# Kernel optimization log

Measured on AMD Instinct MI355X. Metric: run time of the kernel, lower is better.

## Reference

```python
import jax, jax.numpy as jnp
import numpy as np

B, S, D, E, H, TOP_K = 8, 2048, 512, 10, 2048, 2

def setup_inputs() -> dict:
    key = jax.random.key(0)
    ks = jax.random.split(key, 8)
    sd = 0.02
    return {
        "x": jax.random.normal(ks[0], (B, S, D), jnp.float32),
        "noise": jax.random.normal(ks[1], (B, S, E), jnp.float32),
        "Wr": jax.random.normal(ks[2], (D, E), jnp.float32) * sd,
        "br": jnp.zeros((E,), jnp.float32),
        "Wn": jax.random.normal(ks[3], (D, E), jnp.float32) * sd,
        "bn": jnp.zeros((E,), jnp.float32),
        "W1": jax.random.normal(ks[4], (E, D, H), jnp.float32) * sd,
        "b1": jnp.zeros((E, H), jnp.float32),
        "W2": jax.random.normal(ks[5], (E, H, D), jnp.float32) * sd,
        "b2": jnp.zeros((E, D), jnp.float32),
    }

def reference(x, noise, Wr, br, Wn, bn, W1, b1, W2, b2):
    # Noisy top-k router
    logits = x @ Wr + br                                  # [B,S,E]
    noise_logits = x @ Wn + bn                            # [B,S,E]
    noisy = logits + noise * jax.nn.softplus(noise_logits)
    top_vals, top_idx = jax.lax.top_k(noisy, TOP_K)       # [B,S,k]
    # softmax over -inf-scattered logits == softmax over top-k values scattered back
    g_topk = jax.nn.softmax(top_vals, axis=-1)            # [B,S,k]
    n_exp = Wr.shape[-1]
    gating = jnp.sum(jax.nn.one_hot(top_idx, n_exp, dtype=x.dtype) * g_topk[..., None], axis=-2)  # [B,S,E]
    # Dense combine: gating is exactly zero for unselected experts, so weighting
    # every expert's FFN output reproduces the masked gather/scatter loop.
    out = jnp.zeros_like(x)
    for e in range(n_exp):  # small fixed expert count
        h = jax.nn.relu(x @ W1[e] + b1[e])                # [B,S,H]
        y = h @ W2[e] + b2[e]                             # [B,S,D]
        out = out + gating[..., e:e+1] * y
    return out
```

## Files before the change

### kernel.cpp

```cpp
#include <hip/hip_runtime.h>
#include <hip/hip_bf16.h>
#include <stdint.h>


#define N_TOK 16384
#define DIM 512
#define NEXP 10
#define HID 2048
#define BM 128
#define BN 128
#define BK 64
#define MAXSLOT (2*N_TOK + NEXP*BM)
#define NMB (MAXSLOT/BM)
#define RT_TOK 32
#define NBN1 (HID/BN)
#define NBN2 (DIM/BN)

typedef __attribute__((ext_vector_type(8))) short bf16x8;
typedef __attribute__((ext_vector_type(4))) float f32x4;

__device__ __forceinline__ unsigned short f2bf(float v) {
  __hip_bfloat16 h = __float2bfloat16(v);
  return *reinterpret_cast<unsigned short*>(&h);
}

__device__ __forceinline__ void gload_lds16(const void* g, void* l) {
  __builtin_amdgcn_global_load_lds(
      (__attribute__((address_space(1))) void*)g,
      (__attribute__((address_space(3))) void*)l, 16, 0, 0);
}

__device__ __forceinline__ int xcd_chunk(int b, int nwg) {
  int q = nwg >> 3, r = nwg & 7;
  int xcd = b & 7, slot = b >> 3;
  return (xcd < r) ? (xcd*(q+1) + slot) : (r*(q+1) + (xcd-r)*q + slot);
}

__global__ void k_cvt_x(const float* __restrict__ x, unsigned short* __restrict__ xb) {
  size_t i = (size_t)blockIdx.x * 256 + threadIdx.x;
  const float4* xp = (const float4*)x;
  float4 a = xp[2*i], b = xp[2*i+1];
  union { unsigned short us[8]; uint4 u4; } p;
  p.us[0]=f2bf(a.x); p.us[1]=f2bf(a.y); p.us[2]=f2bf(a.z); p.us[3]=f2bf(a.w);
  p.us[4]=f2bf(b.x); p.us[5]=f2bf(b.y); p.us[6]=f2bf(b.z); p.us[7]=f2bf(b.w);
  ((uint4*)xb)[i] = p.u4;
}

__global__ void k_cvt_router_w(const float* __restrict__ Wr, const float* __restrict__ Wn,
                               float* __restrict__ wrt, float* __restrict__ wnt) {
  int i = blockIdx.x * 256 + threadIdx.x;
  if (i < NEXP*DIM) {
    int e = i / DIM, d = i % DIM;
    wrt[i] = Wr[d*NEXP + e];
    wnt[i] = Wn[d*NEXP + e];
  }
}

__global__ void k_transpose(const float* __restrict__ in, unsigned short* __restrict__ outp,
                            int R, int C) {
  __shared__ float tile[64][65];
  int nTR = R >> 6, nTC = C >> 6;
  int b = blockIdx.x;
  int tilesPerE = nTR * nTC;
  int e = b / tilesPerE;
  int t = b % tilesPerE;
  int rb = t / nTC, cb = t % nTC;
  int tr = threadIdx.x >> 6, tc = threadIdx.x & 63;
  const float* ip = in + ((size_t)e*R + (size_t)rb*64) * C + cb*64;
  #pragma unroll
  for (int p = 0; p < 16; ++p)
    tile[p*4 + tr][tc] = ip[(size_t)(p*4 + tr)*C + tc];
  __syncthreads();
  unsigned short* op = outp + ((size_t)e*C + (size_t)cb*64) * R + rb*64;
  int ro = threadIdx.x >> 2;
  int cc = (threadIdx.x & 3) * 16;
  union { unsigned short us[8]; bf16x8 v; } pk;
  #pragma unroll
  for (int half = 0; half < 2; ++half) {
    #pragma unroll
    for (int j = 0; j < 8; ++j) pk.us[j] = f2bf(tile[cc + half*8 + j][ro]);
    *(bf16x8*)&op[(size_t)ro*R + cc + half*8] = pk.v;
  }
}

__global__ __launch_bounds__(256) void k_router2(
    const float* __restrict__ x, const float* __restrict__ noise,
    const float* __restrict__ wrt, const float* __restrict__ wnt,
    const float* __restrict__ br, const float* __restrict__ bnb,
    int* __restrict__ top_idx, float* __restrict__ top_gate, int* __restrict__ counts) {
  __shared__ float part[8][RT_TOK][21];
  __shared__ float red[RT_TOK][21];
  __shared__ float vsh[RT_TOK][10];
  __shared__ int lcnt[16];
  int tid = threadIdx.x;
  int tl = tid & 31;
  int g  = tid >> 5;
  int tok = blockIdx.x * RT_TOK + tl;

  const float4* xr = (const float4*)(x + (size_t)tok*DIM + g*64);
  float acc[20];
  #pragma unroll
  for (int j = 0; j < 20; ++j) acc[j] = 0.f;

  #pragma unroll 4
  for (int c = 0; c < 16; ++c) {
    float4 xv = xr[c];
    int d = g*64 + c*4;
    #pragma unroll
    for (int e = 0; e < NEXP; ++e) {
      float4 a = *(const float4*)(wrt + e*DIM + d);
      float4 b = *(const float4*)(wnt + e*DIM + d);
      acc[e]      += xv.x*a.x + xv.y*a.y + xv.z*a.z + xv.w*a.w;
      acc[10+e]   += xv.x*b.x + xv.y*b.y + xv.z*b.z + xv.w*b.w;
    }
  }
  #pragma unroll
  for (int j = 0; j < 20; ++j) part[g][tl][j] = acc[j];
  __syncthreads();

  for (int o = tid; o < RT_TOK*20; o += 256) {
    int t2 = o / 20, j = o % 20;
    float s = 0.f;
    #pragma unroll
    for (int gg = 0; gg < 8; ++gg) s += part[gg][t2][j];
    red[t2][j] = s;
  }
  __syncthreads();

  for (int o = tid; o < RT_TOK*NEXP; o += 256) {
    int t2 = o / NEXP, e = o % NEXP;
    float nl = red[t2][10+e] + bnb[e];
    float sp = (nl > 20.f) ? nl : log1pf(expf(nl));
    vsh[t2][e] = red[t2][e] + br[e]
               + noise[(size_t)(blockIdx.x*RT_TOK + t2)*NEXP + e] * sp;
  }
  if (tid < 16) lcnt[tid] = 0;
  __syncthreads();

  if (tid < RT_TOK) {
    int t2 = tid;
    float v0 = -1e30f, v1 = -1e30f; int i0 = 0, i1 = 0;
    #pragma unroll
    for (int e = 0; e < NEXP; ++e) {
      float v = vsh[t2][e];
      if (v > v0) { v1 = v0; i1 = i0; v0 = v; i0 = e; }
      else if (v > v1) { v1 = v; i1 = e; }
    }
    float ev = expf(v1 - v0);
    float g0 = 1.f / (1.f + ev);
    float g1 = ev / (1.f + ev);
    int tk = blockIdx.x * RT_TOK + t2;
    top_idx[tk*2] = i0; top_idx[tk*2+1] = i1;
    top_gate[tk*2] = g0; top_gate[tk*2+1] = g1;
    atomicAdd(&lcnt[i0], 1);
    atomicAdd(&lcnt[i1], 1);
  }
  __syncthreads();
  if (tid < NEXP && lcnt[tid] > 0) atomicAdd(&counts[tid], lcnt[tid]);
}

__global__ void k_offsets(const int* __restrict__ counts, int* __restrict__ cursors,
                          int* __restrict__ offs) {
  if (threadIdx.x == 0 && blockIdx.x == 0) {
    int acc = 0;
    for (int e = 0; e < NEXP; ++e) {
      offs[e] = acc; cursors[e] = acc;
      acc += ((counts[e] + BM - 1) / BM) * BM;
    }
    offs[NEXP] = acc;
  }
}

__global__ __launch_bounds__(256) void k_scatter(
    const int* __restrict__ top_idx, const float* __restrict__ top_gate,
    int* __restrict__ cursors, int* __restrict__ slot_token,
    float* __restrict__ slot_gate) {
  __shared__ int lcnt[16];
  __shared__ int lbase[16];
  int tid = threadIdx.x;
  int t = blockIdx.x * 256 + tid;
  if (tid < 16) lcnt[tid] = 0;
  __syncthreads();
  int e0 = top_idx[t*2], e1 = top_idx[t*2+1];
  int r0 = atomicAdd(&lcnt[e0], 1);
  int r1 = atomicAdd(&lcnt[e1], 1);
  __syncthreads();
  if (tid < NEXP && lcnt[tid] > 0) lbase[tid] = atomicAdd(&cursors[tid], lcnt[tid]);
  __syncthreads();
  int p0 = lbase[e0] + r0;
  int p1 = lbase[e1] + r1;
  slot_token[p0] = t; slot_gate[p0] = top_gate[t*2];
  slot_token[p1] = t; slot_gate[p1] = top_gate[t*2+1];
}

__global__ __launch_bounds__(256, 4) void k_gemm1(
    const unsigned short* __restrict__ xb, const unsigned short* __restrict__ w1t,
    const float* __restrict__ b1, const int* __restrict__ slot_token,
    const int* __restrict__ offs, unsigned short* __restrict__ h) {
  __shared__ unsigned short smem[2*BM*BK];
  unsigned short* As = smem;
  unsigned short* Bs = smem + BM*BK;
  int w = xcd_chunk(blockIdx.x, NMB*NBN1);
  int bm = w / NBN1, bn = w % NBN1;
  int tid = threadIdx.x, wid = tid >> 6, lane = tid & 63;
  int s0 = bm * BM;
  int e = 0;
  #pragma unroll
  for (int i = 1; i < NEXP; ++i) if (s0 >= offs[i]) e = i;

  int tokA[4];
  #pragma unroll
  for (int i = 0; i < 4; ++i) {
    int r = (i*4 + wid)*8 + (lane >> 3);
    int t = slot_token[s0 + r];
    tokA[i] = t < 0 ? 0 : t;
  }
  int kcs = ((lane & 7) ^ (lane >> 3)) * 8;
  int ldst = (lane & 7) * 8;
  const unsigned short* w1te = w1t + ((size_t)e*HID + (size_t)bn*BN) * DIM;

  f32x4 acc[4][4];
  #pragma unroll
  for (int m=0;m<4;m++)
    #pragma unroll
    for (int n=0;n<4;n++) acc[m][n] = (f32x4){0.f,0.f,0.f,0.f};

  int wr = wid >> 1, wc = wid & 1;
  int xr = (lane & 7) * 8;

  for (int kt = 0; kt < DIM/BK; ++kt) {
    int k0 = kt * BK;
    #pragma unroll
    for (int i = 0; i < 4; ++i) {
      int r = (i*4 + wid)*8 + (lane >> 3);
      gload_lds16(xb + (size_t)tokA[i]*DIM + k0 + kcs, &As[r*BK + ldst]);
      gload_lds16(w1te + (size_t)r*DIM + k0 + kcs, &Bs[r*BK + ldst]);
    }
    __syncthreads();
    #pragma unroll
    for (int ks = 0; ks < 2; ++ks) {
      int kk = (ks*32 + (lane >> 4)*8) ^ xr;
      bf16x8 a[4], b[4];
      #pragma unroll
      for (int m=0;m<4;m++) a[m] = *(const bf16x8*)&As[(wr*64 + m*16 + (lane&15))*BK + kk];
      #pragma unroll
      for (int n=0;n<4;n++) b[n] = *(const bf16x8*)&Bs[(wc*64 + n*16 + (lane&15))*BK + kk];
      #pragma unroll
      for (int m=0;m<4;m++)
        #pragma unroll
        for (int n=0;n<4;n++)
          acc[m][n] = __builtin_amdgcn_mfma_f32_16x16x32_bf16(a[m], b[n], acc[m][n], 0,0,0);
    }
    __syncthreads();
  }

  unsigned short* ct = smem;
  #pragma unroll
  for (int m=0;m<4;m++){
    int row0 = wr*64 + m*16 + (lane>>4)*4;
    #pragma unroll
    for (int n=0;n<4;n++){
      int lcol = wc*64 + n*16 + (lane&15);
      float bias = b1[e*HID + bn*BN + lcol];
      #pragma unroll
      for (int r=0;r<4;r++){
        int row = row0 + r;
        float v = acc[m][n][r] + bias;
        v = v > 0.f ? v : 0.f;
        int pc = (lcol >> 3) ^ (row & 7);
        ct[row*BN + (pc<<3) + (lcol&7)] = f2bf(v);
      }
    }
  }
  __syncthreads();
  int cchunk = tid & 15, rbase = tid >> 4;
  unsigned short* hb = h + (size_t)s0*HID + bn*BN;
  #pragma unroll
  for (int j=0;j<8;j++){
    int row = rbase + j*16;
    int pc = cchunk ^ (row & 7);
    bf16x8 v = *(const bf16x8*)&ct[row*BN + (pc<<3)];
    *(bf16x8*)&hb[(size_t)row*HID + cchunk*8] = v;
  }
}

__global__ __launch_bounds__(256, 4) void k_gemm2(
    const unsigned short* __restrict__ h, const unsigned short* __restrict__ w2t,
    const float* __restrict__ b2, const int* __restrict__ slot_token,
    const float* __restrict__ slot_gate, const int* __restrict__ offs,
    float* __restrict__ out) {
  __shared__ unsigned short As[BM*BK];
  __shared__ unsigned short Bs[BN*BK];
  int w = xcd_chunk(blockIdx.x, NMB*NBN2);
  int bm = w / NBN2, bn = w % NBN2;
  int tid = threadIdx.x, wid = tid >> 6, lane = tid & 63;
  int s0 = bm * BM;
  int e = 0;
  #pragma unroll
  for (int i = 1; i < NEXP; ++i) if (s0 >= offs[i]) e = i;
  int kcs = ((lane & 7) ^ (lane >> 3)) * 8;
  int ldst = (lane & 7) * 8;
  const unsigned short* w2te = w2t + ((size_t)e*DIM + (size_t)bn*BN) * HID;

  f32x4 acc[4][4];
  #pragma unroll
  for (int m=0;m<4;m++)
    #pragma unroll
    for (int n=0;n<4;n++) acc[m][n] = (f32x4){0.f,0.f,0.f,0.f};

  int wr = wid >> 1, wc = wid & 1;
  int xr = (lane & 7) * 8;

  for (int kt = 0; kt < HID/BK; ++kt) {
    int k0 = kt * BK;
    #pragma unroll
    for (int i = 0; i < 4; ++i) {
      int r = (i*4 + wid)*8 + (lane >> 3);
      gload_lds16(h + (size_t)(s0 + r)*HID + k0 + kcs, &As[r*BK + ldst]);
      gload_lds16(w2te + (size_t)r*HID + k0 + kcs, &Bs[r*BK + ldst]);
    }
    __syncthreads();
    #pragma unroll
    for (int ks = 0; ks < 2; ++ks) {
      int kk = (ks*32 + (lane >> 4)*8) ^ xr;
      bf16x8 a[4], b[4];
      #pragma unroll
      for (int m=0;m<4;m++) a[m] = *(const bf16x8*)&As[(wr*64 + m*16 + (lane&15))*BK + kk];
      #pragma unroll
      for (int n=0;n<4;n++) b[n] = *(const bf16x8*)&Bs[(wc*64 + n*16 + (lane&15))*BK + kk];
      #pragma unroll
      for (int m=0;m<4;m++)
        #pragma unroll
        for (int n=0;n<4;n++)
          acc[m][n] = __builtin_amdgcn_mfma_f32_16x16x32_bf16(a[m], b[n], acc[m][n], 0,0,0);
    }
    __syncthreads();
  }

  #pragma unroll
  for (int m=0;m<4;m++){
    int rb_ = s0 + wr*64 + m*16 + (lane>>4)*4;
    #pragma unroll
    for (int r=0;r<4;r++){
      int slot = rb_ + r;
      int tok = slot_token[slot];
      if (tok < 0) continue;
      float g = slot_gate[slot];
      #pragma unroll
      for (int n=0;n<4;n++){
        int col = bn*BN + wc*64 + n*16 + (lane&15);
        float v = (acc[m][n][r] + b2[e*DIM + col]) * g;
        atomicAdd(&out[(size_t)tok*DIM + col], v);
      }
    }
  }
}

extern "C" void kernel_launch(void* const* d_in, const int* in_sizes, int n_in,
                              void* d_out, int out_size, void* d_ws, size_t ws_size,
                              hipStream_t stream) {
  const float* x   = (const float*)d_in[0];
  const float* noi = (const float*)d_in[1];
  const float* Wr  = (const float*)d_in[2];
  const float* br  = (const float*)d_in[3];
  const float* Wn  = (const float*)d_in[4];
  const float* bnb = (const float*)d_in[5];
  const float* W1  = (const float*)d_in[6];
  const float* b1  = (const float*)d_in[7];
  const float* W2  = (const float*)d_in[8];
  const float* b2  = (const float*)d_in[9];
  float* out = (float*)d_out;
  (void)in_sizes; (void)n_in; (void)ws_size;

  char* ws = (char*)d_ws;
  size_t off = 0;
  auto alloc = [&](size_t bytes) -> void* {
    void* p = ws + off; off += (bytes + 255) & ~(size_t)255; return p;
  };
  unsigned short* w1t  = (unsigned short*)alloc((size_t)NEXP*HID*DIM*2);
  unsigned short* w2t  = (unsigned short*)alloc((size_t)NEXP*DIM*HID*2);
  unsigned short* xb   = (unsigned short*)alloc((size_t)N_TOK*DIM*2);
  unsigned short* hbuf = (unsigned short*)alloc((size_t)MAXSLOT*HID*2);
  float* wrt = (float*)alloc(NEXP*DIM*4);
  float* wnt = (float*)alloc(NEXP*DIM*4);
  int*   top_idx  = (int*)alloc(N_TOK*2*4);
  float* top_gate = (float*)alloc(N_TOK*2*4);
  int*   slot_token = (int*)alloc((size_t)MAXSLOT*4);
  float* slot_gate  = (float*)alloc((size_t)MAXSLOT*4);
  int*   ctrl = (int*)alloc(64*4);
  int* counts  = ctrl;
  int* cursors = ctrl + 10;
  int* offs    = ctrl + 20;

  hipMemsetAsync(out, 0, (size_t)out_size*4, stream);
  hipMemsetAsync(ctrl, 0, 64*4, stream);
  hipMemsetAsync(slot_token, 0xFF, (size_t)MAXSLOT*4, stream);

  k_cvt_x<<<(N_TOK*DIM/8)/256, 256, 0, stream>>>(x, xb);
  k_cvt_router_w<<<(NEXP*DIM+255)/256, 256, 0, stream>>>(Wr, Wn, wrt, wnt);
  k_transpose<<<NEXP*(DIM/64)*(HID/64), 256, 0, stream>>>(W1, w1t, DIM, HID);
  k_transpose<<<NEXP*(HID/64)*(DIM/64), 256, 0, stream>>>(W2, w2t, HID, DIM);
  k_router2<<<N_TOK/RT_TOK, 256, 0, stream>>>(x, noi, wrt, wnt, br, bnb, top_idx, top_gate, counts);
  k_offsets<<<1, 64, 0, stream>>>(counts, cursors, offs);
  k_scatter<<<N_TOK/256, 256, 0, stream>>>(top_idx, top_gate, cursors, slot_token, slot_gate);
  k_gemm1<<<NMB*NBN1, 256, 0, stream>>>(xb, w1t, b1, slot_token, offs, hbuf);
  k_gemm2<<<NMB*NBN2, 256, 0, stream>>>(hbuf, w2t, b2, slot_token, slot_gate, offs, out);
}
```

Measured before the change: 333.2 us.

## Replace atomic scatter in expert GEMM2 with bf16 staging and gather-combine kernel

GEMM2 now writes per-slot expert outputs (plus bias) as bf16 into a staging buffer that reuses the w1t workspace, using coalesced LDS-staged stores instead of per-element fp32 atomicAdds into out. A new combine kernel gathers each token's two slot rows, applies the gate weights and writes out directly, so the output memset is no longer needed. It trades atomic traffic for an extra pass and adds a bf16 rounding of the expert outputs before gating. It also relies on w1t being dead by the time GEMM2 runs.

```diff
diff --git a/kernel.cpp b/kernel.cpp
--- a/kernel.cpp
+++ b/kernel.cpp
@@ -22,6 +22,12 @@
 __device__ __forceinline__ unsigned short f2bf(float v) {
   __hip_bfloat16 h = __float2bfloat16(v);
   return *reinterpret_cast<unsigned short*>(&h);
+}
+
+__device__ __forceinline__ float bf2f(unsigned short u) {
+  union { unsigned int i; float f; } c;
+  c.i = ((unsigned int)u) << 16;
+  return c.f;
 }
 
 __device__ __forceinline__ void gload_lds16(const void* g, void* l) {
@@ -172,9 +178,9 @@
 }
 
 __global__ __launch_bounds__(256) void k_scatter(
-    const int* __restrict__ top_idx, const float* __restrict__ top_gate,
+    const int* __restrict__ top_idx,
     int* __restrict__ cursors, int* __restrict__ slot_token,
-    float* __restrict__ slot_gate) {
+    int* __restrict__ tok_slot) {
   __shared__ int lcnt[16];
   __shared__ int lbase[16];
   int tid = threadIdx.x;
@@ -189,8 +195,10 @@
   __syncthreads();
   int p0 = lbase[e0] + r0;
   int p1 = lbase[e1] + r1;
-  slot_token[p0] = t; slot_gate[p0] = top_gate[t*2];
-  slot_token[p1] = t; slot_gate[p1] = top_gate[t*2+1];
+  slot_token[p0] = t;
+  slot_token[p1] = t;
+  tok_slot[t*2]   = p0;
+  tok_slot[t*2+1] = p1;
 }
 
 __global__ __launch_bounds__(256, 4) void k_gemm1(
@@ -286,11 +294,11 @@
 
 __global__ __launch_bounds__(256, 4) void k_gemm2(
     const unsigned short* __restrict__ h, const unsigned short* __restrict__ w2t,
-    const float* __restrict__ b2, const int* __restrict__ slot_token,
-    const float* __restrict__ slot_gate, const int* __restrict__ offs,
-    float* __restrict__ out) {
-  __shared__ unsigned short As[BM*BK];
-  __shared__ unsigned short Bs[BN*BK];
+    const float* __restrict__ b2, const int* __restrict__ offs,
+    unsigned short* __restrict__ ybuf) {
+  __shared__ unsigned short smem[2*BM*BK];
+  unsigned short* As = smem;
+  unsigned short* Bs = smem + BM*BK;
   int w = xcd_chunk(blockIdx.x, NMB*NBN2);
   int bm = w / NBN2, bn = w % NBN2;
   int tid = threadIdx.x, wid = tid >> 6, lane = tid & 63;
@@ -337,23 +345,53 @@
     __syncthreads();
   }
 
+  unsigned short* ct = smem;
   #pragma unroll
   for (int m=0;m<4;m++){
-    int rb_ = s0 + wr*64 + m*16 + (lane>>4)*4;
-    #pragma unroll
-    for (int r=0;r<4;r++){
-      int slot = rb_ + r;
-      int tok = slot_token[slot];
-      if (tok < 0) continue;
-      float g = slot_gate[slot];
-      #pragma unroll
-      for (int n=0;n<4;n++){
-        int col = bn*BN + wc*64 + n*16 + (lane&15);
-        float v = (acc[m][n][r] + b2[e*DIM + col]) * g;
-        atomicAdd(&out[(size_t)tok*DIM + col], v);
+    int row0 = wr*64 + m*16 + (lane>>4)*4;
+    #pragma unroll
+    for (int n=0;n<4;n++){
+      int lcol = wc*64 + n*16 + (lane&15);
+      float bias = b2[e*DIM + bn*BN + lcol];
+      #pragma unroll
+      for (int r=0;r<4;r++){
+        int row = row0 + r;
+        int pc = (lcol >> 3) ^ (row & 7);
+        ct[row*BN + (pc<<3) + (lcol&7)] = f2bf(acc[m][n][r] + bias);
       }
     }
   }
+  __syncthreads();
+  int cchunk = tid & 15, rbase = tid >> 4;
+  unsigned short* yb = ybuf + (size_t)s0*DIM + bn*BN;
+  #pragma unroll
+  for (int j=0;j<8;j++){
+    int row = rbase + j*16;
+    int pc = cchunk ^ (row & 7);
+    bf16x8 v = *(const bf16x8*)&ct[row*BN + (pc<<3)];
+    *(bf16x8*)&yb[(size_t)row*DIM + cchunk*8] = v;
+  }
+}
+
+__global__ __launch_bounds__(256) void k_combine(
+    const unsigned short* __restrict__ ybuf, const int* __restrict__ tok_slot,
+    const float* __restrict__ top_gate, float* __restrict__ out) {
+  int gid = blockIdx.x * 256 + threadIdx.x;
+  int t = gid >> 6, j = (gid & 63) * 8;
+  int s0 = tok_slot[t*2], s1 = tok_slot[t*2+1];
+  float g0 = top_gate[t*2], g1 = top_gate[t*2+1];
+  union { bf16x8 v; unsigned short us[8]; } y0, y1;
+  y0.v = *(const bf16x8*)&ybuf[(size_t)s0*DIM + j];
+  y1.v = *(const bf16x8*)&ybuf[(size_t)s1*DIM + j];
+  float4 o0, o1;
+  float* op0 = &o0.x;
+  float* op1 = &o1.x;
+  #pragma unroll
+  for (int i = 0; i < 4; ++i) op0[i] = g0*bf2f(y0.us[i])   + g1*bf2f(y1.us[i]);
+  #pragma unroll
+  for (int i = 0; i < 4; ++i) op1[i] = g0*bf2f(y0.us[4+i]) + g1*bf2f(y1.us[4+i]);
+  float4* dst = (float4*)&out[(size_t)t*DIM + j];
+  dst[0] = o0; dst[1] = o1;
 }
 
 extern "C" void kernel_launch(void* const* d_in, const int* in_sizes, int n_in,
@@ -370,7 +408,7 @@
   const float* W2  = (const float*)d_in[8];
   const float* b2  = (const float*)d_in[9];
   float* out = (float*)d_out;
-  (void)in_sizes; (void)n_in; (void)ws_size;
+  (void)in_sizes; (void)n_in; (void)ws_size; (void)out_size;
 
   char* ws = (char*)d_ws;
   size_t off = 0;
@@ -378,21 +416,21 @@
     void* p = ws + off; off += (bytes + 255) & ~(size_t)255; return p;
   };
   unsigned short* w1t  = (unsigned short*)alloc((size_t)NEXP*HID*DIM*2);
+  unsigned short* xb   = (unsigned short*)alloc((size_t)N_TOK*DIM*2);
   unsigned short* w2t  = (unsigned short*)alloc((size_t)NEXP*DIM*HID*2);
-  unsigned short* xb   = (unsigned short*)alloc((size_t)N_TOK*DIM*2);
   unsigned short* hbuf = (unsigned short*)alloc((size_t)MAXSLOT*HID*2);
   float* wrt = (float*)alloc(NEXP*DIM*4);
   float* wnt = (float*)alloc(NEXP*DIM*4);
   int*   top_idx  = (int*)alloc(N_TOK*2*4);
   float* top_gate = (float*)alloc(N_TOK*2*4);
   int*   slot_token = (int*)alloc((size_t)MAXSLOT*4);
-  float* slot_gate  = (float*)alloc((size_t)MAXSLOT*4);
+  int*   tok_slot   = (int*)alloc((size_t)N_TOK*2*4);
   int*   ctrl = (int*)alloc(64*4);
   int* counts  = ctrl;
   int* cursors = ctrl + 10;
   int* offs    = ctrl + 20;
-
-  hipMemsetAsync(out, 0, (size_t)out_size*4, stream);
+  unsigned short* ybuf = w1t;
+
   hipMemsetAsync(ctrl, 0, 64*4, stream);
   hipMemsetAsync(slot_token, 0xFF, (size_t)MAXSLOT*4, stream);
 
@@ -402,7 +440,8 @@
   k_transpose<<<NEXP*(HID/64)*(DIM/64), 256, 0, stream>>>(W2, w2t, HID, DIM);
   k_router2<<<N_TOK/RT_TOK, 256, 0, stream>>>(x, noi, wrt, wnt, br, bnb, top_idx, top_gate, counts);
   k_offsets<<<1, 64, 0, stream>>>(counts, cursors, offs);
-  k_scatter<<<N_TOK/256, 256, 0, stream>>>(top_idx, top_gate, cursors, slot_token, slot_gate);
+  k_scatter<<<N_TOK/256, 256, 0, stream>>>(top_idx, cursors, slot_token, tok_slot);
   k_gemm1<<<NMB*NBN1, 256, 0, stream>>>(xb, w1t, b1, slot_token, offs, hbuf);
-  k_gemm2<<<NMB*NBN2, 256, 0, stream>>>(hbuf, w2t, b2, slot_token, slot_gate, offs, out);
-}
+  k_gemm2<<<NMB*NBN2, 256, 0, stream>>>(hbuf, w2t, b2, offs, ybuf);
+  k_combine<<<(N_TOK*64)/256, 256, 0, stream>>>(ybuf, tok_slot, top_gate, out);
+}
```

Result: faster. 269.4 us (-19.1%).
